# Kernel tuning notes

Measured on AMD Instinct MI355X. Metric: run time of the kernel, lower is better.

## Reference

```python
import jax, jax.numpy as jnp
import numpy as np

N_PAD = 14
N_H = 2 + N_PAD            # 16
N_PAS = 8
MHID = 256
RN = 128
NINF = 128
N_NODES = 50000
N_EDGES = 800000
N_GRAPHS = 500


def setup_inputs() -> dict:
    key = jax.random.key(0)
    ks = jax.random.split(key, 20)
    def g(i, shape, scale=0.1):
        return jax.random.normal(ks[i], shape, jnp.float32) * scale
    return dict(
        x=g(0, (N_NODES, 2), 1.0),
        e=jax.random.uniform(ks[1], (N_EDGES, 1), jnp.float32),
        # edge-matrix MLP l: Dense(Mhid, selu) -> Dense(N_H*N_H) -> reshape
        W_l1=g(2, (1, MHID)), b_l1=jnp.zeros((MHID,), jnp.float32),
        W_l2=g(3, (MHID, N_H * N_H)), b_l2=jnp.zeros((N_H * N_H,), jnp.float32),
        # edge-bias MLP b: Dense(Mhid, selu) -> Dense(N_H)
        W_b1=g(4, (1, MHID)), b_b1=jnp.zeros((MHID,), jnp.float32),
        W_b2=g(5, (MHID, N_H)), b_b2=jnp.zeros((N_H,), jnp.float32),
        # GRUCell (keras default reset_after=True): kernel, recurrent kernel, input/recurrent biases
        gru_Wx=g(6, (N_H, 3 * N_H)), gru_Uh=g(7, (N_H, 3 * N_H)),
        gru_bx=jnp.zeros((3 * N_H,), jnp.float32), gru_bh=jnp.zeros((3 * N_H,), jnp.float32),
        # readout _R on hx = concat([h, x]) with dim N_H + 2
        W_i=g(8, (N_H + 2, RN)), b_i=jnp.zeros((RN,), jnp.float32),
        W_R=g(9, (RN, RN)), b_R=jnp.zeros((RN,), jnp.float32),
        W_j1=g(10, (N_H + 2, RN)), b_j1=jnp.zeros((RN,), jnp.float32),
        W_j2=g(11, (RN, RN)), b_j2=jnp.zeros((RN,), jnp.float32),
        # final head: Dense(ninf, selu) -> Dense(1)
        W_f1=g(12, (RN, NINF)), b_f1=jnp.zeros((NINF,), jnp.float32),
        W_f2=g(13, (NINF, 1)), b_f2=jnp.zeros((1,), jnp.float32),
        first=jax.random.randint(ks[14], (N_EDGES,), 0, N_NODES, jnp.int32),
        second=jax.random.randint(ks[15], (N_EDGES,), 0, N_NODES, jnp.int32),
        segment=jnp.sort(jax.random.randint(ks[16], (N_NODES,), 0, N_GRAPHS, jnp.int32)),
    )


def reference(x, e, W_l1, b_l1, W_l2, b_l2, W_b1, b_b1, W_b2, b_b2,
              gru_Wx, gru_Uh, gru_bx, gru_bh,
              W_i, b_i, W_R, b_R, W_j1, b_j1, W_j2, b_j2,
              W_f1, b_f1, W_f2, b_f2, first, second, segment):
    N = x.shape[0]
    h = jnp.pad(x, ((0, 0), (0, N_PAD)))  # [N, N_H]
    # edge MLPs depend only on e -> hoist out of the message-passing loop (same math)
    a = (jax.nn.selu(e @ W_l1 + b_l1) @ W_l2 + b_l2).reshape(-1, N_H, N_H)  # [E, N_H, N_H]
    be = jax.nn.selu(e @ W_b1 + b_b1) @ W_b2 + b_b2                          # [E, N_H]
    for _ in range(N_PAS):
        hg = h[first]                                    # gather [E, N_H]
        m = jnp.einsum('eij,ej->ei', a, hg) + be         # edge-conditioned matmul
        m = jax.ops.segment_sum(m, second, num_segments=N)  # scatter-add [N, N_H]
        # GRU cell (reset_after=True)
        xz = m @ gru_Wx + gru_bx
        hz = h @ gru_Uh + gru_bh
        xz1, xr1, xh1 = jnp.split(xz, 3, axis=1)
        hz1, hr1, hh1 = jnp.split(hz, 3, axis=1)
        z = jax.nn.sigmoid(xz1 + hz1)
        r = jax.nn.sigmoid(xr1 + hr1)
        hh = jnp.tanh(xh1 + r * hh1)
        h = z * h + (1.0 - z) * hh
    # readout _R
    hx = jnp.concatenate([h, x], axis=1)                  # [N, N_H+2]
    i = jnp.tanh(hx @ W_i + b_i)
    RR = jax.nn.sigmoid(i @ W_R + b_R)
    j = jax.nn.selu(hx @ W_j1 + b_j1) @ W_j2 + b_j2
    nb = jax.ops.segment_sum(RR * j, segment, num_segments=N_GRAPHS)  # [G, RN]
    return jax.nn.selu(nb @ W_f1 + b_f1) @ W_f2 + b_f2    # [G, 1]
```

## Files before the change

kernel.cpp:

```cpp
#include <hip/hip_runtime.h>
#include <math.h>

#define N_NODES  50000
#define N_EDGES  800000
#define N_GRAPHS 500
#define NH       16
#define MHID     256
#define RN       128
#define RO       32
#define NP       5

__device__ __forceinline__ float selu_f(float v) {
    const float scale = 1.0507009873554805f;
    const float alpha = 1.6732632423543772f;
    return v > 0.f ? scale * v : scale * alpha * (expf(v) - 1.f);
}
__device__ __forceinline__ float sigmoid_f(float v) { return 1.f / (1.f + expf(-v)); }

__global__ void build_tables(const float* __restrict__ W_l1, const float* __restrict__ b_l1,
                             const float* __restrict__ W_l2, const float* __restrict__ b_l2,
                             const float* __restrict__ W_b1, const float* __restrict__ b_b1,
                             const float* __restrict__ W_b2, const float* __restrict__ b_b2,
                             float* __restrict__ aT, float* __restrict__ beT) {
    __shared__ float hid[MHID];
    __shared__ float hidb[MHID];
    int t = blockIdx.x;
    int j = threadIdx.x;
    float ev = (float)t / 4.0f;
    hid[j]  = selu_f(ev * W_l1[j] + b_l1[j]);
    hidb[j] = selu_f(ev * W_b1[j] + b_b1[j]);
    __syncthreads();
    float acc = b_l2[j];
    for (int k = 0; k < MHID; ++k)
        acc += hid[k] * W_l2[k * 256 + j];
    aT[t * 256 + j] = acc;
    if (j < NH) {
        float accb = b_b2[j];
        for (int k = 0; k < MHID; ++k)
            accb += hidb[k] * W_b2[k * NH + j];
        beT[t * NH + j] = accb;
    }
}

__global__ void newton_coeffs(const float* __restrict__ aT, const float* __restrict__ beT,
                              float* __restrict__ C, float* __restrict__ beC) {
    int j = threadIdx.x;
    float y[NP];
    #pragma unroll
    for (int k = 0; k < NP; ++k) y[k] = aT[k * 256 + j];
    #pragma unroll
    for (int lvl = 1; lvl < NP; ++lvl)
        #pragma unroll
        for (int k = NP - 1; k >= 1; --k)
            if (k >= lvl) y[k] = (y[k] - y[k - 1]) * (4.0f / (float)lvl);
    #pragma unroll
    for (int p = 0; p < NP; ++p) C[p * 256 + j] = y[p];

    if (j < NH) {
        float z[NP];
        #pragma unroll
        for (int k = 0; k < NP; ++k) z[k] = beT[k * NH + j];
        #pragma unroll
        for (int lvl = 1; lvl < NP; ++lvl)
            #pragma unroll
            for (int k = NP - 1; k >= 1; --k)
                if (k >= lvl) z[k] = (z[k] - z[k - 1]) * (4.0f / (float)lvl);
        #pragma unroll
        for (int p = 0; p < NP; ++p) beC[p * NH + j] = z[p];
    }
}

__global__ void count_deg(const int* __restrict__ second, int* __restrict__ deg) {
    int i = blockIdx.x * blockDim.x + threadIdx.x;
    if (i < N_EDGES) atomicAdd(&deg[second[i]], 1);
}

__global__ void scan1(const int* __restrict__ deg, int* __restrict__ incl, int* __restrict__ bsum) {
    __shared__ int s[256];
    int t = threadIdx.x, i = blockIdx.x * 256 + t;
    int v = (i < N_NODES) ? deg[i] : 0;
    s[t] = v;
    __syncthreads();
    for (int d = 1; d < 256; d <<= 1) {
        int add = (t >= d) ? s[t - d] : 0;
        __syncthreads();
        s[t] += add;
        __syncthreads();
    }
    if (i < N_NODES) incl[i] = s[t];
    if (t == 255) bsum[blockIdx.x] = s[255];
}

__global__ void scan2(const int* __restrict__ bsum, int* __restrict__ bpre, int nblk) {
    __shared__ int s[256];
    int t = threadIdx.x;
    int v = (t < nblk) ? bsum[t] : 0;
    s[t] = v;
    __syncthreads();
    for (int d = 1; d < 256; d <<= 1) {
        int add = (t >= d) ? s[t - d] : 0;
        __syncthreads();
        s[t] += add;
        __syncthreads();
    }
    if (t < nblk) bpre[t] = s[t] - v;
}

__global__ void scan3(const int* __restrict__ incl, const int* __restrict__ deg,
                      const int* __restrict__ bpre, int* __restrict__ off, int* __restrict__ cursor) {
    int i = blockIdx.x * 256 + threadIdx.x;
    if (i < N_NODES) {
        int o = bpre[blockIdx.x] + incl[i] - deg[i];
        off[i] = o;
        cursor[i] = o;
    }
    if (i == 0) off[N_NODES] = N_EDGES;
}

__global__ void sort_hist(const int* __restrict__ deg, int* __restrict__ blockHist) {
    __shared__ int lh[64];
    if (threadIdx.x < 64) lh[threadIdx.x] = 0;
    __syncthreads();
    int i = blockIdx.x * 256 + threadIdx.x;
    if (i < N_NODES) atomicAdd(&lh[min(deg[i], 63)], 1);
    __syncthreads();
    if (threadIdx.x < 64) blockHist[blockIdx.x * 64 + threadIdx.x] = lh[threadIdx.x];
}

__global__ void sort_scan(const int* __restrict__ blockHist, int* __restrict__ blockBase,
                          int* __restrict__ gbase, int nblk) {
    __shared__ int tot[64];
    int b = threadIdx.x;
    int run = 0;
    for (int blk = 0; blk < nblk; ++blk) {
        blockBase[blk * 64 + b] = run;
        run += blockHist[blk * 64 + b];
    }
    tot[b] = run;
    __syncthreads();
    if (b == 0) {
        int acc = 0;
        for (int k = 0; k < 64; ++k) { gbase[k] = acc; acc += tot[k]; }
    }
}

__global__ void sort_rank(const int* __restrict__ deg, const int* __restrict__ blockBase,
                          const int* __restrict__ gbase,
                          int* __restrict__ perm, int* __restrict__ rankOf) {
    __shared__ int bins[256];
    int i = blockIdx.x * 256 + threadIdx.x;
    int b = (i < N_NODES) ? min(deg[i], 63) : -1;
    bins[threadIdx.x] = b;
    __syncthreads();
    if (i < N_NODES) {
        int lr = 0;
        for (int t = 0; t < (int)threadIdx.x; ++t) lr += (bins[t] == b) ? 1 : 0;
        int r = gbase[b] + blockBase[blockIdx.x * 64 + b] + lr;
        perm[r] = i;
        rankOf[i] = r;
    }
}

__global__ void build_rank_init(const int* __restrict__ perm, const int* __restrict__ off,
                                const int* __restrict__ deg, const float* __restrict__ x,
                                int* __restrict__ offR, int* __restrict__ endR,
                                float* __restrict__ h) {
    int r = blockIdx.x * 256 + threadIdx.x;
    if (r >= N_NODES) return;
    int n = perm[r];
    int o = off[n];
    offR[r] = o;
    endR[r] = o + deg[n];
    float4* hp = (float4*)(h + (size_t)r * 16);
    hp[0] = make_float4(x[n * 2 + 0], x[n * 2 + 1], 0.f, 0.f);
    hp[1] = make_float4(0.f, 0.f, 0.f, 0.f);
    hp[2] = make_float4(0.f, 0.f, 0.f, 0.f);
    hp[3] = make_float4(0.f, 0.f, 0.f, 0.f);
}

__global__ void scatter_edges(const float* __restrict__ e, const int* __restrict__ first,
                              const int* __restrict__ second, const int* __restrict__ rankOf,
                              int* __restrict__ cursor, unsigned* __restrict__ em) {
    int i = blockIdx.x * blockDim.x + threadIdx.x;
    if (i >= N_EDGES) return;
    int d = second[i];
    int slot = atomicAdd(&cursor[d], 1);
    unsigned e16 = (unsigned)(e[i] * 65535.f + 0.5f);
    em[slot] = ((unsigned)rankOf[first[i]] << 16) | e16;
}

__global__ __launch_bounds__(256, 4) void mbe_pass(
        const float* __restrict__ beC, const unsigned* __restrict__ em,
        const int* __restrict__ offR, const int* __restrict__ endR,
        float* __restrict__ mBE) {
    int lane = threadIdx.x & 15;
    int grp  = threadIdx.x >> 4;
    int r = blockIdx.x * 16 + grp;
    float c0 = beC[lane], c1 = beC[16 + lane], c2 = beC[32 + lane];
    float c3 = beC[48 + lane], c4 = beC[64 + lane];
    float acc = 0.f;
    int s0 = offR[r], s1 = endR[r];
    for (int base = s0; base < s1; base += 8) {
        unsigned w[8];
        int rem = s1 - base;
        #pragma unroll
        for (int k = 0; k < 8; ++k) w[k] = em[min(base + k, s1 - 1)];
        #pragma unroll
        for (int k = 0; k < 8; ++k) {
            float ev = (float)(w[k] & 0xffffu) * (1.0f / 65535.0f);
            float P = c4;
            P = c3 + (ev - 0.75f) * P;
            P = c2 + (ev - 0.50f) * P;
            P = c1 + (ev - 0.25f) * P;
            P = c0 + ev * P;
            acc += (k < rem) ? P : 0.f;
        }
    }
    mBE[(size_t)r * 16 + lane] = acc;
}

__device__ __forceinline__ void acc_edge(unsigned w, float hv, float msk,
        float& G0, float& G1, float& G2, float& G3, float& G4) {
    float ev = (float)(w & 0xffffu) * (1.0f / 65535.0f);
    float n1 = ev;
    float n2 = n1 * (ev - 0.25f);
    float n3 = n2 * (ev - 0.50f);
    float n4 = n3 * (ev - 0.75f);
    float hm = hv * msk;
    G0 += hm; G1 += n1 * hm; G2 += n2 * hm; G3 += n3 * hm; G4 += n4 * hm;
}

__global__ __launch_bounds__(256, 4) void edge_gru(
        const float* __restrict__ Cg, const unsigned* __restrict__ em,
        const int* __restrict__ offR, const int* __restrict__ endR,
        const float* __restrict__ mBE,
        const float* __restrict__ hOld, float* __restrict__ hNew,
        const float* __restrict__ Wx, const float* __restrict__ Uh,
        const float* __restrict__ bx, const float* __restrict__ bh) {
    __shared__ float sC[NP][16][17];
    __shared__ float sWx[768], sUh[768], sb[96];
    __shared__ float sG[16][NP][16];
    __shared__ float sm[16][16], sh[16][16];

    for (int i = threadIdx.x; i < NP * 256; i += 256) {
        int p = i >> 8, jj = i & 255;
        sC[p][jj >> 4][jj & 15] = Cg[i];
    }
    for (int i = threadIdx.x; i < 768; i += 256) { sWx[i] = Wx[i]; sUh[i] = Uh[i]; }
    if (threadIdx.x < 96)
        sb[threadIdx.x] = (threadIdx.x < 48) ? bx[threadIdx.x] : bh[threadIdx.x - 48];
    __syncthreads();

    int lane = threadIdx.x & 15;
    int grp  = threadIdx.x >> 4;
    int r = blockIdx.x * 16 + grp;
    float hn = hOld[(size_t)r * 16 + lane];
    sh[grp][lane] = hn;

    int s0 = offR[r], s1 = endR[r];
    float G0 = 0.f, G1 = 0.f, G2 = 0.f, G3 = 0.f, G4 = 0.f;

    if (s0 < s1) {
        unsigned w0[4];
        float hv0[4];
        #pragma unroll
        for (int k = 0; k < 4; ++k) w0[k] = em[min(s0 + k, s1 - 1)];
        #pragma unroll
        for (int k = 0; k < 4; ++k)
            hv0[k] = hOld[(size_t)(w0[k] >> 16) * 16 + lane];

        for (int base = s0; base < s1; base += 4) {
            int nbase = base + 4;
            unsigned w1[4];
            float hv1[4];
            #pragma unroll
            for (int k = 0; k < 4; ++k)
                w1[k] = em[(nbase < s1) ? min(nbase + k, s1 - 1) : base];
            #pragma unroll
            for (int k = 0; k < 4; ++k)
                hv1[k] = hOld[(size_t)(w1[k] >> 16) * 16 + lane];

            int rem = base == s0 ? (s1 - base) : (s1 - base);
            #pragma unroll
            for (int k = 0; k < 4; ++k)
                acc_edge(w0[k], hv0[k], (k < rem) ? 1.f : 0.f, G0, G1, G2, G3, G4);

            #pragma unroll
            for (int k = 0; k < 4; ++k) { w0[k] = w1[k]; hv0[k] = hv1[k]; }
        }
    }

    sG[grp][0][lane] = G0; sG[grp][1][lane] = G1; sG[grp][2][lane] = G2;
    sG[grp][3][lane] = G3; sG[grp][4][lane] = G4;

    float mi = mBE[(size_t)r * 16 + lane];
    #pragma unroll
    for (int p = 0; p < NP; ++p) {
        #pragma unroll
        for (int k = 0; k < 16; ++k)
            mi += sC[p][lane][k] * sG[grp][p][k];
    }
    sm[grp][lane] = mi;

    float xz = sb[lane], xr = sb[16 + lane], xh = sb[32 + lane];
    float hz = sb[48 + lane], hr = sb[64 + lane], hhp = sb[80 + lane];
    #pragma unroll
    for (int k = 0; k < 16; ++k) {
        float mk = sm[grp][k], hk = sh[grp][k];
        xz  += mk * sWx[k * 48 + lane];
        xr  += mk * sWx[k * 48 + 16 + lane];
        xh  += mk * sWx[k * 48 + 32 + lane];
        hz  += hk * sUh[k * 48 + lane];
        hr  += hk * sUh[k * 48 + 16 + lane];
        hhp += hk * sUh[k * 48 + 32 + lane];
    }
    float z  = sigmoid_f(xz + hz);
    float rr = sigmoid_f(xr + hr);
    float hc = tanhf(xh + rr * hhp);
    hNew[(size_t)r * 16 + lane] = z * hn + (1.f - z) * hc;
}

__global__ __launch_bounds__(256) void readout(
        const float* __restrict__ h, const float* __restrict__ x,
        const int* __restrict__ segment, const int* __restrict__ rankOf,
        const float* __restrict__ W_i, const float* __restrict__ b_i,
        const float* __restrict__ W_R, const float* __restrict__ b_R,
        const float* __restrict__ W_j1, const float* __restrict__ b_j1,
        const float* __restrict__ W_j2, const float* __restrict__ b_j2,
        float* __restrict__ nb) {
    __shared__ float hx[RO][19];
    __shared__ __align__(16) float ilT[RN][36];
    __shared__ __align__(16) float jlT[RN][36];
    __shared__ int seg[RO], rnk[RO];
    float (*sRR)[132] = (float (*)[132]) & ilT[0][0];

    int node0 = blockIdx.x * RO;
    int tid = threadIdx.x;

    if (tid < RO) {
        int nd = node0 + tid;
        rnk[tid] = (nd < N_NODES) ? rankOf[nd] : 0;
        seg[tid] = segment[min(nd, N_NODES - 1)];
    }
    __syncthreads();

    for (int idx = tid; idx < RO * 18; idx += 256) {
        int n = idx / 18, k = idx % 18;
        int nd = node0 + n;
        float v = 0.f;
        if (nd < N_NODES)
            v = (k < 16) ? h[(size_t)rnk[n] * 16 + k] : x[(size_t)nd * 2 + (k - 16)];
        hx[n][k] = v;
    }
    __syncthreads();

    int j = tid & 127, half = tid >> 7;
    {
        const float* W1 = half ? W_j1 : W_i;
        float bv = half ? b_j1[j] : b_i[j];
        #pragma unroll 1
        for (int ch = 0; ch < 2; ++ch) {
            float acc[16];
            #pragma unroll
            for (int n = 0; n < 16; ++n) acc[n] = bv;
            for (int k = 0; k < 18; ++k) {
                float w = W1[k * RN + j];
                #pragma unroll
                for (int n = 0; n < 16; ++n)
                    acc[n] += hx[(ch * 16 + n + j) & 31][k] * w;
            }
            if (half == 0) {
                #pragma unroll
                for (int n = 0; n < 16; ++n)
                    ilT[j][(ch * 16 + n + j) & 31] = tanhf(acc[n]);
            } else {
                #pragma unroll
                for (int n = 0; n < 16; ++n)
                    jlT[j][(ch * 16 + n + j) & 31] = selu_f(acc[n]);
            }
        }
    }
    __syncthreads();

    int cg = tid & 31, ngp = tid >> 5;
    int j0 = cg * 4, n0 = ngp * 4;

    {
        float4 bR4 = *(const float4*)&b_R[j0];
        float aR[4][4];
        #pragma unroll
        for (int n = 0; n < 4; ++n) {
            aR[n][0] = bR4.x; aR[n][1] = bR4.y; aR[n][2] = bR4.z; aR[n][3] = bR4.w;
        }
        #pragma unroll 2
        for (int k = 0; k < RN; ++k) {
            float4 wr = *(const float4*)&W_R[k * RN + j0];
            float4 iv = *(const float4*)&ilT[k][n0];
            float ivv[4] = {iv.x, iv.y, iv.z, iv.w};
            float wrv[4] = {wr.x, wr.y, wr.z, wr.w};
            #pragma unroll
            for (int n = 0; n < 4; ++n)
                #pragma unroll
                for (int c = 0; c < 4; ++c)
                    aR[n][c] += ivv[n] * wrv[c];
        }
        __syncthreads();
        #pragma unroll
        for (int n = 0; n < 4; ++n)
            #pragma unroll
            for (int c = 0; c < 4; ++c)
                sRR[n0 + n][j0 + c] = sigmoid_f(aR[n][c]);
    }

    float4 bj4 = *(const float4*)&b_j2[j0];
    float aJ[4][4];
    #pragma unroll
    for (int n = 0; n < 4; ++n) {
        aJ[n][0] = bj4.x; aJ[n][1] = bj4.y; aJ[n][2] = bj4.z; aJ[n][3] = bj4.w;
    }
    #pragma unroll 2
    for (int k = 0; k < RN; ++k) {
        float4 wj = *(const float4*)&W_j2[k * RN + j0];
        float4 jv = *(const float4*)&jlT[k][n0];
        float jvv[4] = {jv.x, jv.y, jv.z, jv.w};
        float wjv[4] = {wj.x, wj.y, wj.z, wj.w};
        #pragma unroll
        for (int n = 0; n < 4; ++n)
            #pragma unroll
            for (int c = 0; c < 4; ++c)
                aJ[n][c] += jvv[n] * wjv[c];
    }

    float f0 = 0.f, f1 = 0.f, f2 = 0.f, f3 = 0.f;
    int cur = seg[n0];
    #pragma unroll
    for (int n = 0; n < 4; ++n) {
        int sg = seg[n0 + n];
        if (sg != cur) {
            atomicAdd(&nb[(size_t)cur * RN + j0 + 0], f0);
            atomicAdd(&nb[(size_t)cur * RN + j0 + 1], f1);
            atomicAdd(&nb[(size_t)cur * RN + j0 + 2], f2);
            atomicAdd(&nb[(size_t)cur * RN + j0 + 3], f3);
            f0 = f1 = f2 = f3 = 0.f;
            cur = sg;
        }
        float vm = (node0 + n0 + n < N_NODES) ? 1.f : 0.f;
        f0 += vm * sRR[n0 + n][j0 + 0] * aJ[n][0];
        f1 += vm * sRR[n0 + n][j0 + 1] * aJ[n][1];
        f2 += vm * sRR[n0 + n][j0 + 2] * aJ[n][2];
        f3 += vm * sRR[n0 + n][j0 + 3] * aJ[n][3];
    }
    atomicAdd(&nb[(size_t)cur * RN + j0 + 0], f0);
    atomicAdd(&nb[(size_t)cur * RN + j0 + 1], f1);
    atomicAdd(&nb[(size_t)cur * RN + j0 + 2], f2);
    atomicAdd(&nb[(size_t)cur * RN + j0 + 3], f3);
}

__global__ void final_head(const float* __restrict__ nb, const float* __restrict__ W_f1,
                           const float* __restrict__ b_f1, const float* __restrict__ W_f2,
                           const float* __restrict__ b_f2, float* __restrict__ out) {
    __shared__ float row[128];
    __shared__ float red[128];
    int g = blockIdx.x, j = threadIdx.x;
    row[j] = nb[(size_t)g * 128 + j];
    __syncthreads();
    float a = b_f1[j];
    for (int k = 0; k < 128; ++k)
        a += row[k] * W_f1[k * 128 + j];
    red[j] = selu_f(a) * W_f2[j];
    __syncthreads();
    for (int s2 = 64; s2 > 0; s2 >>= 1) {
        if (j < s2) red[j] += red[j + s2];
        __syncthreads();
    }
    if (j == 0) out[g] = red[0] + b_f2[0];
}

extern "C" void kernel_launch(void* const* d_in, const int* in_sizes, int n_in,
                              void* d_out, int out_size, void* d_ws, size_t ws_size,
                              hipStream_t stream) {
    const float* x    = (const float*)d_in[0];
    const float* e    = (const float*)d_in[1];
    const float* W_l1 = (const float*)d_in[2];
    const float* b_l1 = (const float*)d_in[3];
    const float* W_l2 = (const float*)d_in[4];
    const float* b_l2 = (const float*)d_in[5];
    const float* W_b1 = (const float*)d_in[6];
    const float* b_b1 = (const float*)d_in[7];
    const float* W_b2 = (const float*)d_in[8];
    const float* b_b2 = (const float*)d_in[9];
    const float* gWx  = (const float*)d_in[10];
    const float* gUh  = (const float*)d_in[11];
    const float* gbx  = (const float*)d_in[12];
    const float* gbh  = (const float*)d_in[13];
    const float* W_i  = (const float*)d_in[14];
    const float* b_i  = (const float*)d_in[15];
    const float* W_R  = (const float*)d_in[16];
    const float* b_R  = (const float*)d_in[17];
    const float* W_j1 = (const float*)d_in[18];
    const float* b_j1 = (const float*)d_in[19];
    const float* W_j2 = (const float*)d_in[20];
    const float* b_j2 = (const float*)d_in[21];
    const float* W_f1 = (const float*)d_in[22];
    const float* b_f1 = (const float*)d_in[23];
    const float* W_f2 = (const float*)d_in[24];
    const float* b_f2 = (const float*)d_in[25];
    const int* first   = (const int*)d_in[26];
    const int* second  = (const int*)d_in[27];
    const int* segment = (const int*)d_in[28];
    float* out = (float*)d_out;

    float* ws    = (float*)d_ws;
    float* aT    = ws;
    float* beT   = aT + 1280;
    float* Cg    = beT + 80;
    float* beC   = Cg + 1280;
    float* mBE   = beC + 80;
    float* hA    = mBE + 800000;
    float* hB    = hA + 800000;
    float* nb    = hB + 800000;
    int*   deg   = (int*)(nb + 64000);
    int*   incl  = deg + N_NODES;
    int*   off   = incl + N_NODES;
    int*   cur   = off + N_NODES + 1;
    int*   bsum  = cur + N_NODES;
    int*   bpre  = bsum + 256;
    int*   perm  = bpre + 256;
    int*   rankOf= perm + N_NODES;
    int*   offR  = rankOf + N_NODES;
    int*   endR  = offR + N_NODES;
    int*   blockHist = endR + N_NODES;
    int*   blockBase = blockHist + 12544;
    int*   gbase = blockBase + 12544;
    unsigned* em = (unsigned*)(gbase + 64);

    const int NBLK = (N_NODES + 255) / 256;

    build_tables<<<NP, 256, 0, stream>>>(W_l1, b_l1, W_l2, b_l2,
                                         W_b1, b_b1, W_b2, b_b2, aT, beT);
    newton_coeffs<<<1, 256, 0, stream>>>(aT, beT, Cg, beC);

    hipMemsetAsync(deg, 0, N_NODES * sizeof(int), stream);
    count_deg<<<N_EDGES / 256, 256, 0, stream>>>(second, deg);
    scan1<<<NBLK, 256, 0, stream>>>(deg, incl, bsum);
    scan2<<<1, 256, 0, stream>>>(bsum, bpre, NBLK);
    scan3<<<NBLK, 256, 0, stream>>>(incl, deg, bpre, off, cur);
    sort_hist<<<NBLK, 256, 0, stream>>>(deg, blockHist);
    sort_scan<<<1, 64, 0, stream>>>(blockHist, blockBase, gbase, NBLK);
    sort_rank<<<NBLK, 256, 0, stream>>>(deg, blockBase, gbase, perm, rankOf);
    build_rank_init<<<NBLK, 256, 0, stream>>>(perm, off, deg, x, offR, endR, hA);
    scatter_edges<<<N_EDGES / 256, 256, 0, stream>>>(e, first, second, rankOf, cur, em);
    mbe_pass<<<N_NODES / 16, 256, 0, stream>>>(beC, em, offR, endR, mBE);

    float* hc = hA;
    float* hn = hB;
    for (int p = 0; p < 8; ++p) {
        edge_gru<<<N_NODES / 16, 256, 0, stream>>>(Cg, em, offR, endR, mBE,
                                                   hc, hn, gWx, gUh, gbx, gbh);
        float* tmp = hc; hc = hn; hn = tmp;
    }

    hipMemsetAsync(nb, 0, (size_t)N_GRAPHS * 128 * sizeof(float), stream);
    readout<<<(N_NODES + RO - 1) / RO, 256, 0, stream>>>(
        hc, x, segment, rankOf, W_i, b_i, W_R, b_R, W_j1, b_j1, W_j2, b_j2, nb);
    final_head<<<N_GRAPHS, 128, 0, stream>>>(nb, W_f1, b_f1, W_f2, b_f2, out);
}
```

Measured before the change: 533.7 us.

## Process two node tiles per edge_gru block and register-tile readout first layer

edge_gru now handles 32 nodes per block in two passes, halving grid size so the shared-memory setup of coefficient and GRU weights is amortized over more nodes. The edge loop switches from a 4-wide software-pipelined prefetch to 8-wide batches with a full-batch fast path and a masked tail. In readout, the first dense layer is recomputed with a 4x4 register tile using float4 weight loads instead of the per-column loop, and a sync is added before the second GEMM. The changes trade per-block parallelism and cross-iteration prefetch for amortized setup and more loads in flight.

```diff
diff --git a/kernel.cpp b/kernel.cpp
--- a/kernel.cpp
+++ b/kernel.cpp
@@ -253,71 +253,73 @@
 
     int lane = threadIdx.x & 15;
     int grp  = threadIdx.x >> 4;
-    int r = blockIdx.x * 16 + grp;
-    float hn = hOld[(size_t)r * 16 + lane];
-    sh[grp][lane] = hn;
-
-    int s0 = offR[r], s1 = endR[r];
-    float G0 = 0.f, G1 = 0.f, G2 = 0.f, G3 = 0.f, G4 = 0.f;
-
-    if (s0 < s1) {
-        unsigned w0[4];
-        float hv0[4];
-        #pragma unroll
-        for (int k = 0; k < 4; ++k) w0[k] = em[min(s0 + k, s1 - 1)];
-        #pragma unroll
-        for (int k = 0; k < 4; ++k)
-            hv0[k] = hOld[(size_t)(w0[k] >> 16) * 16 + lane];
-
-        for (int base = s0; base < s1; base += 4) {
-            int nbase = base + 4;
-            unsigned w1[4];
-            float hv1[4];
-            #pragma unroll
-            for (int k = 0; k < 4; ++k)
-                w1[k] = em[(nbase < s1) ? min(nbase + k, s1 - 1) : base];
-            #pragma unroll
-            for (int k = 0; k < 4; ++k)
-                hv1[k] = hOld[(size_t)(w1[k] >> 16) * 16 + lane];
-
-            int rem = base == s0 ? (s1 - base) : (s1 - base);
-            #pragma unroll
-            for (int k = 0; k < 4; ++k)
-                acc_edge(w0[k], hv0[k], (k < rem) ? 1.f : 0.f, G0, G1, G2, G3, G4);
-
-            #pragma unroll
-            for (int k = 0; k < 4; ++k) { w0[k] = w1[k]; hv0[k] = hv1[k]; }
-        }
-    }
-
-    sG[grp][0][lane] = G0; sG[grp][1][lane] = G1; sG[grp][2][lane] = G2;
-    sG[grp][3][lane] = G3; sG[grp][4][lane] = G4;
-
-    float mi = mBE[(size_t)r * 16 + lane];
-    #pragma unroll
-    for (int p = 0; p < NP; ++p) {
-        #pragma unroll
-        for (int k = 0; k < 16; ++k)
-            mi += sC[p][lane][k] * sG[grp][p][k];
-    }
-    sm[grp][lane] = mi;
-
-    float xz = sb[lane], xr = sb[16 + lane], xh = sb[32 + lane];
-    float hz = sb[48 + lane], hr = sb[64 + lane], hhp = sb[80 + lane];
-    #pragma unroll
-    for (int k = 0; k < 16; ++k) {
-        float mk = sm[grp][k], hk = sh[grp][k];
-        xz  += mk * sWx[k * 48 + lane];
-        xr  += mk * sWx[k * 48 + 16 + lane];
-        xh  += mk * sWx[k * 48 + 32 + lane];
-        hz  += hk * sUh[k * 48 + lane];
-        hr  += hk * sUh[k * 48 + 16 + lane];
-        hhp += hk * sUh[k * 48 + 32 + lane];
-    }
-    float z  = sigmoid_f(xz + hz);
-    float rr = sigmoid_f(xr + hr);
-    float hc = tanhf(xh + rr * hhp);
-    hNew[(size_t)r * 16 + lane] = z * hn + (1.f - z) * hc;
+
+    #pragma unroll 1
+    for (int t = 0; t < 2; ++t) {
+        int r = blockIdx.x * 32 + t * 16 + grp;
+        int rc = min(r, N_NODES - 1);
+        float hn = hOld[(size_t)rc * 16 + lane];
+        sh[grp][lane] = hn;
+
+        int s0 = offR[rc], s1 = endR[rc];
+        float G0 = 0.f, G1 = 0.f, G2 = 0.f, G3 = 0.f, G4 = 0.f;
+
+        for (int base = s0; base < s1; base += 8) {
+            const unsigned* p = em + base;
+            unsigned w[8];
+            float hv[8];
+            if (base + 8 <= s1) {
+                #pragma unroll
+                for (int k = 0; k < 8; ++k) w[k] = p[k];
+                #pragma unroll
+                for (int k = 0; k < 8; ++k)
+                    hv[k] = hOld[(size_t)(w[k] >> 16) * 16 + lane];
+                #pragma unroll
+                for (int k = 0; k < 8; ++k)
+                    acc_edge(w[k], hv[k], 1.f, G0, G1, G2, G3, G4);
+            } else {
+                int rem = s1 - base;
+                #pragma unroll
+                for (int k = 0; k < 8; ++k) w[k] = p[min(k, rem - 1)];
+                #pragma unroll
+                for (int k = 0; k < 8; ++k)
+                    hv[k] = hOld[(size_t)(w[k] >> 16) * 16 + lane];
+                #pragma unroll
+                for (int k = 0; k < 8; ++k)
+                    acc_edge(w[k], hv[k], (k < rem) ? 1.f : 0.f, G0, G1, G2, G3, G4);
+            }
+        }
+
+        sG[grp][0][lane] = G0; sG[grp][1][lane] = G1; sG[grp][2][lane] = G2;
+        sG[grp][3][lane] = G3; sG[grp][4][lane] = G4;
+
+        float mi = mBE[(size_t)rc * 16 + lane];
+        #pragma unroll
+        for (int p = 0; p < NP; ++p) {
+            #pragma unroll
+            for (int k = 0; k < 16; ++k)
+                mi += sC[p][lane][k] * sG[grp][p][k];
+        }
+        sm[grp][lane] = mi;
+
+        float xz = sb[lane], xr = sb[16 + lane], xh = sb[32 + lane];
+        float hz = sb[48 + lane], hr = sb[64 + lane], hhp = sb[80 + lane];
+        #pragma unroll
+        for (int k = 0; k < 16; ++k) {
+            float mk = sm[grp][k], hk = sh[grp][k];
+            xz  += mk * sWx[k * 48 + lane];
+            xr  += mk * sWx[k * 48 + 16 + lane];
+            xh  += mk * sWx[k * 48 + 32 + lane];
+            hz  += hk * sUh[k * 48 + lane];
+            hr  += hk * sUh[k * 48 + 16 + lane];
+            hhp += hk * sUh[k * 48 + 32 + lane];
+        }
+        float z  = sigmoid_f(xz + hz);
+        float rr = sigmoid_f(xr + hr);
+        float hc = tanhf(xh + rr * hhp);
+        if (r < N_NODES)
+            hNew[(size_t)r * 16 + lane] = z * hn + (1.f - z) * hc;
+    }
 }
 
 __global__ __launch_bounds__(256) void readout(
@@ -354,36 +356,57 @@
     }
     __syncthreads();
 
-    int j = tid & 127, half = tid >> 7;
-    {
-        const float* W1 = half ? W_j1 : W_i;
-        float bv = half ? b_j1[j] : b_i[j];
-        #pragma unroll 1
-        for (int ch = 0; ch < 2; ++ch) {
-            float acc[16];
-            #pragma unroll
-            for (int n = 0; n < 16; ++n) acc[n] = bv;
-            for (int k = 0; k < 18; ++k) {
-                float w = W1[k * RN + j];
-                #pragma unroll
-                for (int n = 0; n < 16; ++n)
-                    acc[n] += hx[(ch * 16 + n + j) & 31][k] * w;
-            }
-            if (half == 0) {
-                #pragma unroll
-                for (int n = 0; n < 16; ++n)
-                    ilT[j][(ch * 16 + n + j) & 31] = tanhf(acc[n]);
-            } else {
-                #pragma unroll
-                for (int n = 0; n < 16; ++n)
-                    jlT[j][(ch * 16 + n + j) & 31] = selu_f(acc[n]);
-            }
-        }
-    }
-    __syncthreads();
-
     int cg = tid & 31, ngp = tid >> 5;
     int j0 = cg * 4, n0 = ngp * 4;
+
+    {
+        float4 b4 = *(const float4*)&b_i[j0];
+        float a[4][4];
+        #pragma unroll
+        for (int n = 0; n < 4; ++n) {
+            a[n][0] = b4.x; a[n][1] = b4.y; a[n][2] = b4.z; a[n][3] = b4.w;
+        }
+        for (int k = 0; k < 18; ++k) {
+            float4 w = *(const float4*)&W_i[k * RN + j0];
+            float wv[4] = {w.x, w.y, w.z, w.w};
+            float hv[4] = {hx[n0 + 0][k], hx[n0 + 1][k], hx[n0 + 2][k], hx[n0 + 3][k]};
+            #pragma unroll
+            for (int n = 0; n < 4; ++n)
+                #pragma unroll
+                for (int c = 0; c < 4; ++c)
+                    a[n][c] += hv[n] * wv[c];
+        }
+        #pragma unroll
+        for (int n = 0; n < 4; ++n)
+            #pragma unroll
+            for (int c = 0; c < 4; ++c)
+                ilT[j0 + c][n0 + n] = tanhf(a[n][c]);
+    }
+
+    {
+        float4 b4 = *(const float4*)&b_j1[j0];
+        float a[4][4];
+        #pragma unroll
+        for (int n = 0; n < 4; ++n) {
+            a[n][0] = b4.x; a[n][1] = b4.y; a[n][2] = b4.z; a[n][3] = b4.w;
+        }
+        for (int k = 0; k < 18; ++k) {
+            float4 w = *(const float4*)&W_j1[k * RN + j0];
+            float wv[4] = {w.x, w.y, w.z, w.w};
+            float hv[4] = {hx[n0 + 0][k], hx[n0 + 1][k], hx[n0 + 2][k], hx[n0 + 3][k]};
+            #pragma unroll
+            for (int n = 0; n < 4; ++n)
+                #pragma unroll
+                for (int c = 0; c < 4; ++c)
+                    a[n][c] += hv[n] * wv[c];
+        }
+        #pragma unroll
+        for (int n = 0; n < 4; ++n)
+            #pragma unroll
+            for (int c = 0; c < 4; ++c)
+                jlT[j0 + c][n0 + n] = selu_f(a[n][c]);
+    }
+    __syncthreads();
 
     {
         float4 bR4 = *(const float4*)&b_R[j0];
@@ -411,6 +434,7 @@
             for (int c = 0; c < 4; ++c)
                 sRR[n0 + n][j0 + c] = sigmoid_f(aR[n][c]);
     }
+    __syncthreads();
 
     float4 bj4 = *(const float4*)&b_j2[j0];
     float aJ[4][4];
@@ -554,9 +578,10 @@
 
     float* hc = hA;
     float* hn = hB;
+    const int EGRID = (N_NODES + 31) / 32;
     for (int p = 0; p < 8; ++p) {
-        edge_gru<<<N_NODES / 16, 256, 0, stream>>>(Cg, em, offR, endR, mBE,
-                                                   hc, hn, gWx, gUh, gbx, gbh);
+        edge_gru<<<EGRID, 256, 0, stream>>>(Cg, em, offR, endR, mBE,
+                                            hc, hn, gWx, gUh, gbx, gbh);
         float* tmp = hc; hc = hn; hn = tmp;
     }
 
```

Result: slower. 1.225 ms (+129.5%).
